# Performance work log

Measured on AMD Instinct MI355X. Metric: run time of the kernel, lower is better.

## Reference

```python
import jax, jax.numpy as jnp
import numpy as np


def _graph_conv_mean(x, src, dst, edge_weight, W_rel, W_root, b, num_nodes):
    # messages: gather source features, optionally scale by edge weight
    msg = x[src]  # [E, D]
    if edge_weight is not None:
        msg = msg * edge_weight[:, None]
    # mean aggregation over incoming edges per destination node
    summed = jax.ops.segment_sum(msg, dst, num_segments=num_nodes)  # [N, D]
    count = jax.ops.segment_sum(jnp.ones((src.shape[0],), x.dtype), dst, num_segments=num_nodes)
    mean = summed / jnp.maximum(count, 1.0)[:, None]
    # out = lin_rel(mean) + lin_root(x) + bias
    return mean @ W_rel + x @ W_root + b


def setup_inputs() -> dict:
    key = jax.random.key(0)
    ks = jax.random.split(key, 8)
    N, E, D, H, C = 100000, 1600000, 128, 32, 5
    x = jax.random.normal(ks[0], (N, D), dtype=jnp.float32)
    edge_index = jax.random.randint(ks[1], (2, E), 0, N, dtype=jnp.int64)
    edge_weight = jax.random.uniform(ks[2], (E,), dtype=jnp.float32)
    W_rel1 = jax.random.normal(ks[3], (D, H), dtype=jnp.float32) / np.sqrt(D)
    W_root1 = jax.random.normal(ks[4], (D, H), dtype=jnp.float32) / np.sqrt(D)
    b1 = jnp.zeros((H,), jnp.float32)
    W_rel2 = jax.random.normal(ks[5], (H, C), dtype=jnp.float32) / np.sqrt(H)
    W_root2 = jax.random.normal(ks[6], (H, C), dtype=jnp.float32) / np.sqrt(H)
    b2 = jnp.zeros((C,), jnp.float32)
    return {"x": x, "edge_index": edge_index, "edge_weight": edge_weight,
            "W_rel1": W_rel1, "W_root1": W_root1, "b1": b1,
            "W_rel2": W_rel2, "W_root2": W_root2, "b2": b2}


def reference(x, edge_index, edge_weight, W_rel1, W_root1, b1, W_rel2, W_root2, b2):
    N = x.shape[0]
    src, dst = edge_index[0], edge_index[1]
    # conv1 with edge_weight
    h = _graph_conv_mean(x, src, dst, edge_weight, W_rel1, W_root1, b1, N)
    h = jax.nn.relu(h)
    # dropout is identity at inference (training=False)
    # conv2 without edge_weight
    out = _graph_conv_mean(h, src, dst, None, W_rel2, W_root2, b2, N)
    return jax.nn.log_softmax(out, axis=1)
```

## Files before the change

kernel.cpp:

```cpp
#include <hip/hip_runtime.h>
#include <math.h>

#define N_NODES 100000
#define E_EDGES 1600000
#define D_IN    128
#define H_MID   32
#define C_OUT   5

#define BSHIFT 9
#define BNODES 512
#define NBKT   196
#define BCAP   9200
#define SRC_BITS 17
#define SRC_MASK 0x1FFFF

#define KP 136

typedef __attribute__((ext_vector_type(8))) short bf16x8;
typedef __attribute__((ext_vector_type(4))) float f32x4;

__device__ inline unsigned f2bf(float f) {
    unsigned u = __float_as_uint(f);
    return (u + 0x7FFFu + ((u >> 16) & 1u)) >> 16;
}

__global__ void k_prep(const float* __restrict__ Wrel,
                       const float* __restrict__ Wroot,
                       int* __restrict__ bucket_cursor,
                       unsigned short* __restrict__ wt_g) {
    int tid = threadIdx.x;
    bucket_cursor[tid] = 0;
    for (int i = tid; i < 64 * 128; i += 256) {
        int n = i >> 7, k = i & 127;
        float v = (n < H_MID) ? Wrel[k * H_MID + n] : Wroot[k * H_MID + (n - H_MID)];
        wt_g[i] = (unsigned short)f2bf(v);
    }
}

__global__ __launch_bounds__(256) void k1_mfma(
    const float* __restrict__ x,
    const unsigned short* __restrict__ wt_g,
    const float* __restrict__ b1,
    unsigned short* __restrict__ xrelh,
    float* __restrict__ xroot) {
    __shared__ unsigned short xs[64 * KP];
    int tid = threadIdx.x;
    int nodeBase = blockIdx.x * 64;

    #pragma unroll
    for (int it = 0; it < 16; ++it) {
        int idx = it * 256 + tid;
        int row = idx >> 6, kp = idx & 63;
        int node = nodeBase + row;
        float2 v = make_float2(0.f, 0.f);
        if (node < N_NODES)
            v = *(const float2*)(x + (size_t)node * D_IN + kp * 2);
        unsigned pk = f2bf(v.x) | (f2bf(v.y) << 16);
        *(unsigned*)(xs + row * KP + kp * 2) = pk;
    }
    __syncthreads();

    int lane = tid & 63;
    int wv = tid >> 6;
    int m = lane & 15;
    int quad = lane >> 4;

    f32x4 acc[4];
    #pragma unroll
    for (int nt = 0; nt < 4; ++nt) acc[nt] = (f32x4){0.f, 0.f, 0.f, 0.f};

    #pragma unroll
    for (int kk = 0; kk < 4; ++kk) {
        int k0 = kk * 32 + quad * 8;
        bf16x8 a = *(const bf16x8*)(xs + (wv * 16 + m) * KP + k0);
        #pragma unroll
        for (int nt = 0; nt < 4; ++nt) {
            bf16x8 b = *(const bf16x8*)(wt_g + (nt * 16 + m) * 128 + k0);
            acc[nt] = __builtin_amdgcn_mfma_f32_16x16x32_bf16(a, b, acc[nt], 0, 0, 0);
        }
    }

    #pragma unroll
    for (int nt = 0; nt < 4; ++nt) {
        #pragma unroll
        for (int r = 0; r < 4; ++r) {
            int node = nodeBase + wv * 16 + quad * 4 + r;
            int colg = nt * 16 + m;
            if (node < N_NODES) {
                if (colg < H_MID) {
                    xrelh[(size_t)node * H_MID + colg] =
                        (unsigned short)f2bf(acc[nt][r]);
                } else {
                    int c = colg - H_MID;
                    xroot[(size_t)node * H_MID + c] = acc[nt][r] + b1[c];
                }
            }
        }
    }
}

__global__ __launch_bounds__(1024) void k_binA(
    const int* __restrict__ src,
    const int* __restrict__ dst,
    const float* __restrict__ ew,
    int* __restrict__ bucket_cursor,
    int2* __restrict__ staged) {
    __shared__ int cnt[NBKT];
    __shared__ int lstart[NBKT];
    __shared__ int gbase[NBKT];
    __shared__ int scanbuf[256];
    __shared__ int2 ebuf[2048];
    __shared__ short bbuf[2048];
    int tid = threadIdx.x;
    int eBase = blockIdx.x * 2048;

    if (tid < NBKT) cnt[tid] = 0;
    __syncthreads();

    int b[2], rank[2], packed[2], wbits[2];
    bool valid[2];
    #pragma unroll
    for (int u = 0; u < 2; ++u) {
        int e = eBase + u * 1024 + tid;
        valid[u] = (e < E_EDGES);
        b[u] = 0; rank[u] = 0; packed[u] = 0; wbits[u] = 0;
        if (valid[u]) {
            int d = dst[e];
            int s = src[e];
            wbits[u] = __float_as_int(ew[e]);
            b[u] = d >> BSHIFT;
            packed[u] = ((d & (BNODES - 1)) << SRC_BITS) | s;
            rank[u] = atomicAdd(&cnt[b[u]], 1);
        }
    }
    __syncthreads();

    if (tid < 256) scanbuf[tid] = (tid < NBKT) ? cnt[tid] : 0;
    __syncthreads();
    for (int off = 1; off < 256; off <<= 1) {
        int t = 0;
        if (tid < 256 && tid >= off) t = scanbuf[tid - off];
        __syncthreads();
        if (tid < 256) scanbuf[tid] += t;
        __syncthreads();
    }
    if (tid < NBKT) {
        lstart[tid] = scanbuf[tid] - cnt[tid];
        gbase[tid]  = atomicAdd(&bucket_cursor[tid], cnt[tid]);
    }
    __syncthreads();
    int total = scanbuf[NBKT - 1];

    #pragma unroll
    for (int u = 0; u < 2; ++u) {
        if (valid[u]) {
            int slot = lstart[b[u]] + rank[u];
            ebuf[slot] = make_int2(packed[u], wbits[u]);
            bbuf[slot] = (short)b[u];
        }
    }
    __syncthreads();

    for (int t = tid; t < total; t += 1024) {
        int2 ev = ebuf[t];
        int bb = bbuf[t];
        int gpos = gbase[bb] + (t - lstart[bb]);
        if (gpos < BCAP)
            staged[(size_t)bb * BCAP + gpos] = ev;
    }
}

__global__ __launch_bounds__(1024) void k_binB2(
    const int* __restrict__ bucket_cursor,
    const int2* __restrict__ staged,
    int* __restrict__ deg,
    int* __restrict__ offsets,
    int2* __restrict__ csr8) {
    __shared__ int hist[BNODES];
    __shared__ int scanb[BNODES];
    __shared__ int cur[BNODES];
    __shared__ int sbase[256];
    int tid = threadIdx.x;
    int b = blockIdx.x;

    if (tid < 256) {
        int c = (tid < NBKT) ? bucket_cursor[tid] : 0;
        sbase[tid] = (c > BCAP) ? BCAP : c;
    }
    if (tid < BNODES) hist[tid] = 0;
    __syncthreads();
    for (int off = 1; off < 256; off <<= 1) {
        int t = 0;
        if (tid < 256 && tid >= off) t = sbase[tid - off];
        __syncthreads();
        if (tid < 256) sbase[tid] += t;
        __syncthreads();
    }
    int count = bucket_cursor[b];
    if (count > BCAP) count = BCAP;
    int base = sbase[b] - count;
    int nodeBase = b << BSHIFT;
    const int2* sp = staged + (size_t)b * BCAP;

    for (int i = tid; i < count; i += 1024)
        atomicAdd(&hist[((unsigned)sp[i].x) >> SRC_BITS], 1);
    __syncthreads();

    int v = 0;
    if (tid < BNODES) {
        v = hist[tid];
        scanb[tid] = v;
    }
    __syncthreads();
    for (int off = 1; off < BNODES; off <<= 1) {
        int t = 0;
        if (tid < BNODES && tid >= off) t = scanb[tid - off];
        __syncthreads();
        if (tid < BNODES) scanb[tid] += t;
        __syncthreads();
    }
    if (tid < BNODES) {
        int excl = scanb[tid] - v;
        int node = nodeBase + tid;
        if (node < N_NODES) {
            deg[node]     = v;
            offsets[node] = base + excl;
        }
        cur[tid] = excl;
    }
    __syncthreads();

    for (int i = tid; i < count; i += 1024) {
        int2 ev = sp[i];
        int local = ((unsigned)ev.x) >> SRC_BITS;
        int pos = atomicAdd(&cur[local], 1);
        csr8[base + pos] = make_int2(ev.x & SRC_MASK, ev.y);
    }
}

__global__ __launch_bounds__(512) void k_layer1(
    const int* __restrict__ offsets,
    const int* __restrict__ deg,
    const int2* __restrict__ csr8,
    const unsigned short* __restrict__ xrelh,
    const float* __restrict__ xroot,
    const float* __restrict__ Wrel2,
    const float* __restrict__ Wroot2,
    const float* __restrict__ b2,
    float* __restrict__ h2rel,
    float* __restrict__ h2root) {
    int node = blockIdx.x * 32 + (threadIdx.x >> 4);
    int lane = threadIdx.x & 15;
    int beg = offsets[node];
    int dg  = deg[node];
    int end = beg + dg;

    float acc0 = 0.f, acc1 = 0.f;
    int i = beg;
    for (; i + 8 <= end; i += 8) {
        int2 e[8];
        unsigned v[8];
        #pragma unroll
        for (int u = 0; u < 8; ++u) e[u] = csr8[i + u];
        #pragma unroll
        for (int u = 0; u < 8; ++u)
            v[u] = *(const unsigned*)(xrelh + (size_t)e[u].x * H_MID + lane * 2);
        #pragma unroll
        for (int u = 0; u < 8; ++u) {
            float w = __int_as_float(e[u].y);
            acc0 += __uint_as_float((v[u] & 0xFFFFu) << 16) * w;
            acc1 += __uint_as_float(v[u] & 0xFFFF0000u) * w;
        }
    }
    for (; i < end; ++i) {
        int2 e0 = csr8[i];
        unsigned v0 = *(const unsigned*)(xrelh + (size_t)e0.x * H_MID + lane * 2);
        float w0 = __int_as_float(e0.y);
        acc0 += __uint_as_float((v0 & 0xFFFFu) << 16) * w0;
        acc1 += __uint_as_float(v0 & 0xFFFF0000u) * w0;
    }

    float inv = 1.0f / fmaxf((float)dg, 1.0f);
    float2 rt = *(const float2*)(xroot + (size_t)node * H_MID + lane * 2);
    float h0 = fmaxf(acc0 * inv + rt.x, 0.f);
    float h1 = fmaxf(acc1 * inv + rt.y, 0.f);

    float p[2 * C_OUT];
    #pragma unroll
    for (int j = 0; j < C_OUT; ++j) {
        p[j]         = h0 * Wrel2[(2 * lane) * C_OUT + j]
                     + h1 * Wrel2[(2 * lane + 1) * C_OUT + j];
        p[C_OUT + j] = h0 * Wroot2[(2 * lane) * C_OUT + j]
                     + h1 * Wroot2[(2 * lane + 1) * C_OUT + j];
    }
    #pragma unroll
    for (int mm = 8; mm > 0; mm >>= 1) {
        #pragma unroll
        for (int j = 0; j < 2 * C_OUT; ++j)
            p[j] += __shfl_xor(p[j], mm, 16);
    }
    if (lane == 0) {
        #pragma unroll
        for (int j = 0; j < C_OUT; ++j) {
            h2rel[(size_t)node * C_OUT + j]  = p[j];
            h2root[(size_t)node * C_OUT + j] = p[C_OUT + j] + b2[j];
        }
    }
}

__global__ __launch_bounds__(256) void k_layer2(
    const int* __restrict__ offsets,
    const int* __restrict__ deg,
    const int2* __restrict__ csr8,
    const float* __restrict__ h2rel,
    const float* __restrict__ h2root,
    float* __restrict__ out) {
    int node = blockIdx.x * 32 + (threadIdx.x >> 3);
    int lane = threadIdx.x & 7;
    int beg = offsets[node];
    int dg  = deg[node];
    int end = beg + dg;

    float acc = 0.f;
    if (lane < C_OUT) {
        int i = beg;
        for (; i + 8 <= end; i += 8) {
            int s[8];
            float v[8];
            #pragma unroll
            for (int u = 0; u < 8; ++u) s[u] = csr8[i + u].x;
            #pragma unroll
            for (int u = 0; u < 8; ++u)
                v[u] = h2rel[(size_t)s[u] * C_OUT + lane];
            #pragma unroll
            for (int u = 0; u < 8; ++u) acc += v[u];
        }
        for (; i < end; ++i)
            acc += h2rel[(size_t)csr8[i].x * C_OUT + lane];
    }
    float inv = 1.0f / fmaxf((float)dg, 1.0f);
    float o = (lane < C_OUT)
                  ? acc * inv + h2root[(size_t)node * C_OUT + lane]
                  : -INFINITY;
    float m = o;
    #pragma unroll
    for (int dd = 4; dd > 0; dd >>= 1) m = fmaxf(m, __shfl_xor(m, dd, 8));
    float e = (lane < C_OUT) ? expf(o - m) : 0.f;
    float ssum = e;
    #pragma unroll
    for (int dd = 4; dd > 0; dd >>= 1) ssum += __shfl_xor(ssum, dd, 8);
    float lse = m + logf(ssum);
    if (lane < C_OUT)
        out[(size_t)node * C_OUT + lane] = o - lse;
}

extern "C" void kernel_launch(void* const* d_in, const int* in_sizes, int n_in,
                              void* d_out, int out_size, void* d_ws, size_t ws_size,
                              hipStream_t stream) {
    const float* x      = (const float*)d_in[0];
    const int*   ei     = (const int*)d_in[1];
    const float* ew     = (const float*)d_in[2];
    const float* Wrel1  = (const float*)d_in[3];
    const float* Wroot1 = (const float*)d_in[4];
    const float* b1     = (const float*)d_in[5];
    const float* Wrel2  = (const float*)d_in[6];
    const float* Wroot2 = (const float*)d_in[7];
    const float* b2     = (const float*)d_in[8];
    float* out = (float*)d_out;

    const int* src = ei;
    const int* dst = ei + E_EDGES;

    char* ws = (char*)d_ws;
    int*   deg           = (int*)ws;
    int*   bucket_cursor = deg + N_NODES;
    unsigned short* wt_g = (unsigned short*)(bucket_cursor + 256);
    int*   offsets       = (int*)(wt_g + 64 * 128);
    int2*  csr8          = (int2*)(offsets + N_NODES);
    unsigned short* xrelh = (unsigned short*)(csr8 + E_EDGES);
    float* xroot         = (float*)(xrelh + (size_t)N_NODES * H_MID);
    float* h2rel         = xroot + (size_t)N_NODES * H_MID;
    float* h2root        = h2rel + (size_t)N_NODES * C_OUT;
    int2*  staged        = (int2*)xrelh;

    k_prep<<<1, 256, 0, stream>>>(Wrel1, Wroot1, bucket_cursor, wt_g);

    k_binA<<<(E_EDGES + 2047) / 2048, 1024, 0, stream>>>(src, dst, ew,
                                                         bucket_cursor, staged);
    k_binB2<<<NBKT, 1024, 0, stream>>>(bucket_cursor, staged,
                                       deg, offsets, csr8);

    k1_mfma<<<(N_NODES + 63) / 64, 256, 0, stream>>>(x, wt_g, b1,
                                                     xrelh, xroot);

    k_layer1<<<N_NODES / 32, 512, 0, stream>>>(offsets, deg, csr8,
                                               xrelh, xroot, Wrel2, Wroot2, b2,
                                               h2rel, h2root);

    k_layer2<<<N_NODES / 32, 256, 0, stream>>>(offsets, deg, csr8,
                                               h2rel, h2root, out);
}
```

Before: 224.3 us.

## Fuse edge binning with node GEMM and aggregate per bucket from LDS CSR

Merges the edge-binning pass and the MFMA node-transform into one launch by splitting block ranges, and removes the global CSR build. Each layer kernel now re-sorts its bucket's staged edges into shared memory and aggregates directly from LDS, so the global csr/offset/deg arrays and one launch disappear. Bucket size halves to 256 nodes, giving 391 buckets and more blocks in the per-bucket kernels. The cost is that the per-bucket sort is done twice, once per layer, and the front kernel needs more shared memory per block with a wider scan.

```diff
diff --git a/kernel.cpp b/kernel.cpp
--- a/kernel.cpp
+++ b/kernel.cpp
@@ -7,12 +7,16 @@
 #define H_MID   32
 #define C_OUT   5
 
-#define BSHIFT 9
-#define BNODES 512
-#define NBKT   196
-#define BCAP   9200
+#define BSHIFT 8
+#define BNODES 256
+#define NBKT   391
+#define BCAP   4500
 #define SRC_BITS 17
 #define SRC_MASK 0x1FFFF
+
+#define EB     2048
+#define NBA    782
+#define NMF    782
 
 #define KP 136
 
@@ -23,6 +27,8 @@
     unsigned u = __float_as_uint(f);
     return (u + 0x7FFFu + ((u >> 16) & 1u)) >> 16;
 }
+__device__ inline float bflo(unsigned v) { return __uint_as_float((v & 0xFFFFu) << 16); }
+__device__ inline float bfhi(unsigned v) { return __uint_as_float(v & 0xFFFF0000u); }
 
 __global__ void k_prep(const float* __restrict__ Wrel,
                        const float* __restrict__ Wroot,
@@ -30,218 +36,152 @@
                        unsigned short* __restrict__ wt_g) {
     int tid = threadIdx.x;
     bucket_cursor[tid] = 0;
-    for (int i = tid; i < 64 * 128; i += 256) {
+    for (int i = tid; i < 64 * 128; i += 512) {
         int n = i >> 7, k = i & 127;
         float v = (n < H_MID) ? Wrel[k * H_MID + n] : Wroot[k * H_MID + (n - H_MID)];
         wt_g[i] = (unsigned short)f2bf(v);
     }
 }
 
-__global__ __launch_bounds__(256) void k1_mfma(
+__global__ __launch_bounds__(1024) void k_front(
+    const int* __restrict__ src,
+    const int* __restrict__ dst,
+    const float* __restrict__ ew,
+    int* __restrict__ bucket_cursor,
+    int2* __restrict__ staged,
     const float* __restrict__ x,
     const unsigned short* __restrict__ wt_g,
     const float* __restrict__ b1,
     unsigned short* __restrict__ xrelh,
     float* __restrict__ xroot) {
-    __shared__ unsigned short xs[64 * KP];
+    __shared__ __align__(16) char smem[128 * KP * 2];
     int tid = threadIdx.x;
-    int nodeBase = blockIdx.x * 64;
-
-    #pragma unroll
-    for (int it = 0; it < 16; ++it) {
-        int idx = it * 256 + tid;
-        int row = idx >> 6, kp = idx & 63;
-        int node = nodeBase + row;
-        float2 v = make_float2(0.f, 0.f);
-        if (node < N_NODES)
-            v = *(const float2*)(x + (size_t)node * D_IN + kp * 2);
-        unsigned pk = f2bf(v.x) | (f2bf(v.y) << 16);
-        *(unsigned*)(xs + row * KP + kp * 2) = pk;
-    }
-    __syncthreads();
-
-    int lane = tid & 63;
-    int wv = tid >> 6;
-    int m = lane & 15;
-    int quad = lane >> 4;
-
-    f32x4 acc[4];
-    #pragma unroll
-    for (int nt = 0; nt < 4; ++nt) acc[nt] = (f32x4){0.f, 0.f, 0.f, 0.f};
-
-    #pragma unroll
-    for (int kk = 0; kk < 4; ++kk) {
-        int k0 = kk * 32 + quad * 8;
-        bf16x8 a = *(const bf16x8*)(xs + (wv * 16 + m) * KP + k0);
-        #pragma unroll
-        for (int nt = 0; nt < 4; ++nt) {
-            bf16x8 b = *(const bf16x8*)(wt_g + (nt * 16 + m) * 128 + k0);
-            acc[nt] = __builtin_amdgcn_mfma_f32_16x16x32_bf16(a, b, acc[nt], 0, 0, 0);
-        }
-    }
-
-    #pragma unroll
-    for (int nt = 0; nt < 4; ++nt) {
-        #pragma unroll
-        for (int r = 0; r < 4; ++r) {
-            int node = nodeBase + wv * 16 + quad * 4 + r;
-            int colg = nt * 16 + m;
-            if (node < N_NODES) {
-                if (colg < H_MID) {
-                    xrelh[(size_t)node * H_MID + colg] =
-                        (unsigned short)f2bf(acc[nt][r]);
-                } else {
-                    int c = colg - H_MID;
-                    xroot[(size_t)node * H_MID + c] = acc[nt][r] + b1[c];
+
+    if (blockIdx.x < NBA) {
+        int2*  ebuf    = (int2*)smem;
+        short* bbuf    = (short*)(smem + 16384);
+        int*   cnt     = (int*)(smem + 20480);
+        int*   lstart  = (int*)(smem + 22080);
+        int*   gbase   = (int*)(smem + 23680);
+        int*   scanbuf = (int*)(smem + 25280);
+        int eBase = blockIdx.x * EB;
+
+        if (tid < NBKT) cnt[tid] = 0;
+        __syncthreads();
+
+        int b[2], rank[2], packed[2], wbits[2];
+        bool valid[2];
+        #pragma unroll
+        for (int u = 0; u < 2; ++u) {
+            int e = eBase + u * 1024 + tid;
+            valid[u] = (e < E_EDGES);
+            b[u] = 0; rank[u] = 0; packed[u] = 0; wbits[u] = 0;
+            if (valid[u]) {
+                int d = dst[e];
+                int s = src[e];
+                wbits[u] = __float_as_int(ew[e]);
+                b[u] = d >> BSHIFT;
+                packed[u] = ((d & (BNODES - 1)) << SRC_BITS) | s;
+                rank[u] = atomicAdd(&cnt[b[u]], 1);
+            }
+        }
+        __syncthreads();
+
+        if (tid < 512) scanbuf[tid] = (tid < NBKT) ? cnt[tid] : 0;
+        __syncthreads();
+        for (int off = 1; off < 512; off <<= 1) {
+            int t = 0;
+            if (tid < 512 && tid >= off) t = scanbuf[tid - off];
+            __syncthreads();
+            if (tid < 512) scanbuf[tid] += t;
+            __syncthreads();
+        }
+        if (tid < NBKT) {
+            lstart[tid] = scanbuf[tid] - cnt[tid];
+            gbase[tid]  = atomicAdd(&bucket_cursor[tid], cnt[tid]);
+        }
+        __syncthreads();
+        int total = scanbuf[NBKT - 1];
+
+        #pragma unroll
+        for (int u = 0; u < 2; ++u) {
+            if (valid[u]) {
+                int slot = lstart[b[u]] + rank[u];
+                ebuf[slot] = make_int2(packed[u], wbits[u]);
+                bbuf[slot] = (short)b[u];
+            }
+        }
+        __syncthreads();
+
+        for (int t = tid; t < total; t += 1024) {
+            int2 ev = ebuf[t];
+            int bb = bbuf[t];
+            int gpos = gbase[bb] + (t - lstart[bb]);
+            if (gpos < BCAP)
+                staged[(size_t)bb * BCAP + gpos] = ev;
+        }
+    } else {
+        unsigned short* xs = (unsigned short*)smem;
+        int nodeBase = (blockIdx.x - NBA) * 128;
+
+        #pragma unroll
+        for (int it = 0; it < 8; ++it) {
+            int idx = it * 1024 + tid;
+            int row = idx >> 6, kp = idx & 63;
+            int node = nodeBase + row;
+            float2 v = make_float2(0.f, 0.f);
+            if (node < N_NODES)
+                v = *(const float2*)(x + (size_t)node * D_IN + kp * 2);
+            unsigned pk = f2bf(v.x) | (f2bf(v.y) << 16);
+            *(unsigned*)(xs + row * KP + kp * 2) = pk;
+        }
+        __syncthreads();
+
+        int lane = tid & 63;
+        int wv = tid >> 6;
+        int m = lane & 15;
+        int quad = lane >> 4;
+        int rowBase = (wv & 7) * 16;
+        int ntBase = (wv >> 3) * 2;
+
+        f32x4 acc[2];
+        acc[0] = (f32x4){0.f, 0.f, 0.f, 0.f};
+        acc[1] = (f32x4){0.f, 0.f, 0.f, 0.f};
+
+        #pragma unroll
+        for (int kk = 0; kk < 4; ++kk) {
+            int k0 = kk * 32 + quad * 8;
+            bf16x8 a = *(const bf16x8*)(xs + (rowBase + m) * KP + k0);
+            #pragma unroll
+            for (int t = 0; t < 2; ++t) {
+                bf16x8 bb = *(const bf16x8*)(wt_g + ((ntBase + t) * 16 + m) * 128 + k0);
+                acc[t] = __builtin_amdgcn_mfma_f32_16x16x32_bf16(a, bb, acc[t], 0, 0, 0);
+            }
+        }
+
+        #pragma unroll
+        for (int t = 0; t < 2; ++t) {
+            #pragma unroll
+            for (int r = 0; r < 4; ++r) {
+                int node = nodeBase + rowBase + quad * 4 + r;
+                int colg = (ntBase + t) * 16 + m;
+                if (node < N_NODES) {
+                    if (colg < H_MID) {
+                        xrelh[(size_t)node * H_MID + colg] =
+                            (unsigned short)f2bf(acc[t][r]);
+                    } else {
+                        int c = colg - H_MID;
+                        xroot[(size_t)node * H_MID + c] = acc[t][r] + b1[c];
+                    }
                 }
             }
         }
     }
 }
 
-__global__ __launch_bounds__(1024) void k_binA(
-    const int* __restrict__ src,
-    const int* __restrict__ dst,
-    const float* __restrict__ ew,
-    int* __restrict__ bucket_cursor,
-    int2* __restrict__ staged) {
-    __shared__ int cnt[NBKT];
-    __shared__ int lstart[NBKT];
-    __shared__ int gbase[NBKT];
-    __shared__ int scanbuf[256];
-    __shared__ int2 ebuf[2048];
-    __shared__ short bbuf[2048];
-    int tid = threadIdx.x;
-    int eBase = blockIdx.x * 2048;
-
-    if (tid < NBKT) cnt[tid] = 0;
-    __syncthreads();
-
-    int b[2], rank[2], packed[2], wbits[2];
-    bool valid[2];
-    #pragma unroll
-    for (int u = 0; u < 2; ++u) {
-        int e = eBase + u * 1024 + tid;
-        valid[u] = (e < E_EDGES);
-        b[u] = 0; rank[u] = 0; packed[u] = 0; wbits[u] = 0;
-        if (valid[u]) {
-            int d = dst[e];
-            int s = src[e];
-            wbits[u] = __float_as_int(ew[e]);
-            b[u] = d >> BSHIFT;
-            packed[u] = ((d & (BNODES - 1)) << SRC_BITS) | s;
-            rank[u] = atomicAdd(&cnt[b[u]], 1);
-        }
-    }
-    __syncthreads();
-
-    if (tid < 256) scanbuf[tid] = (tid < NBKT) ? cnt[tid] : 0;
-    __syncthreads();
-    for (int off = 1; off < 256; off <<= 1) {
-        int t = 0;
-        if (tid < 256 && tid >= off) t = scanbuf[tid - off];
-        __syncthreads();
-        if (tid < 256) scanbuf[tid] += t;
-        __syncthreads();
-    }
-    if (tid < NBKT) {
-        lstart[tid] = scanbuf[tid] - cnt[tid];
-        gbase[tid]  = atomicAdd(&bucket_cursor[tid], cnt[tid]);
-    }
-    __syncthreads();
-    int total = scanbuf[NBKT - 1];
-
-    #pragma unroll
-    for (int u = 0; u < 2; ++u) {
-        if (valid[u]) {
-            int slot = lstart[b[u]] + rank[u];
-            ebuf[slot] = make_int2(packed[u], wbits[u]);
-            bbuf[slot] = (short)b[u];
-        }
-    }
-    __syncthreads();
-
-    for (int t = tid; t < total; t += 1024) {
-        int2 ev = ebuf[t];
-        int bb = bbuf[t];
-        int gpos = gbase[bb] + (t - lstart[bb]);
-        if (gpos < BCAP)
-            staged[(size_t)bb * BCAP + gpos] = ev;
-    }
-}
-
-__global__ __launch_bounds__(1024) void k_binB2(
+__global__ __launch_bounds__(1024) void k_bucket1(
     const int* __restrict__ bucket_cursor,
     const int2* __restrict__ staged,
-    int* __restrict__ deg,
-    int* __restrict__ offsets,
-    int2* __restrict__ csr8) {
-    __shared__ int hist[BNODES];
-    __shared__ int scanb[BNODES];
-    __shared__ int cur[BNODES];
-    __shared__ int sbase[256];
-    int tid = threadIdx.x;
-    int b = blockIdx.x;
-
-    if (tid < 256) {
-        int c = (tid < NBKT) ? bucket_cursor[tid] : 0;
-        sbase[tid] = (c > BCAP) ? BCAP : c;
-    }
-    if (tid < BNODES) hist[tid] = 0;
-    __syncthreads();
-    for (int off = 1; off < 256; off <<= 1) {
-        int t = 0;
-        if (tid < 256 && tid >= off) t = sbase[tid - off];
-        __syncthreads();
-        if (tid < 256) sbase[tid] += t;
-        __syncthreads();
-    }
-    int count = bucket_cursor[b];
-    if (count > BCAP) count = BCAP;
-    int base = sbase[b] - count;
-    int nodeBase = b << BSHIFT;
-    const int2* sp = staged + (size_t)b * BCAP;
-
-    for (int i = tid; i < count; i += 1024)
-        atomicAdd(&hist[((unsigned)sp[i].x) >> SRC_BITS], 1);
-    __syncthreads();
-
-    int v = 0;
-    if (tid < BNODES) {
-        v = hist[tid];
-        scanb[tid] = v;
-    }
-    __syncthreads();
-    for (int off = 1; off < BNODES; off <<= 1) {
-        int t = 0;
-        if (tid < BNODES && tid >= off) t = scanb[tid - off];
-        __syncthreads();
-        if (tid < BNODES) scanb[tid] += t;
-        __syncthreads();
-    }
-    if (tid < BNODES) {
-        int excl = scanb[tid] - v;
-        int node = nodeBase + tid;
-        if (node < N_NODES) {
-            deg[node]     = v;
-            offsets[node] = base + excl;
-        }
-        cur[tid] = excl;
-    }
-    __syncthreads();
-
-    for (int i = tid; i < count; i += 1024) {
-        int2 ev = sp[i];
-        int local = ((unsigned)ev.x) >> SRC_BITS;
-        int pos = atomicAdd(&cur[local], 1);
-        csr8[base + pos] = make_int2(ev.x & SRC_MASK, ev.y);
-    }
-}
-
-__global__ __launch_bounds__(512) void k_layer1(
-    const int* __restrict__ offsets,
-    const int* __restrict__ deg,
-    const int2* __restrict__ csr8,
     const unsigned short* __restrict__ xrelh,
     const float* __restrict__ xroot,
     const float* __restrict__ Wrel2,
@@ -249,109 +189,194 @@
     const float* __restrict__ b2,
     float* __restrict__ h2rel,
     float* __restrict__ h2root) {
-    int node = blockIdx.x * 32 + (threadIdx.x >> 4);
-    int lane = threadIdx.x & 15;
-    int beg = offsets[node];
-    int dg  = deg[node];
-    int end = beg + dg;
-
-    float acc0 = 0.f, acc1 = 0.f;
-    int i = beg;
-    for (; i + 8 <= end; i += 8) {
-        int2 e[8];
-        unsigned v[8];
-        #pragma unroll
-        for (int u = 0; u < 8; ++u) e[u] = csr8[i + u];
-        #pragma unroll
-        for (int u = 0; u < 8; ++u)
-            v[u] = *(const unsigned*)(xrelh + (size_t)e[u].x * H_MID + lane * 2);
-        #pragma unroll
-        for (int u = 0; u < 8; ++u) {
-            float w = __int_as_float(e[u].y);
-            acc0 += __uint_as_float((v[u] & 0xFFFFu) << 16) * w;
-            acc1 += __uint_as_float(v[u] & 0xFFFF0000u) * w;
-        }
-    }
-    for (; i < end; ++i) {
-        int2 e0 = csr8[i];
-        unsigned v0 = *(const unsigned*)(xrelh + (size_t)e0.x * H_MID + lane * 2);
-        float w0 = __int_as_float(e0.y);
-        acc0 += __uint_as_float((v0 & 0xFFFFu) << 16) * w0;
-        acc1 += __uint_as_float(v0 & 0xFFFF0000u) * w0;
-    }
-
-    float inv = 1.0f / fmaxf((float)dg, 1.0f);
-    float2 rt = *(const float2*)(xroot + (size_t)node * H_MID + lane * 2);
-    float h0 = fmaxf(acc0 * inv + rt.x, 0.f);
-    float h1 = fmaxf(acc1 * inv + rt.y, 0.f);
-
-    float p[2 * C_OUT];
-    #pragma unroll
-    for (int j = 0; j < C_OUT; ++j) {
-        p[j]         = h0 * Wrel2[(2 * lane) * C_OUT + j]
-                     + h1 * Wrel2[(2 * lane + 1) * C_OUT + j];
-        p[C_OUT + j] = h0 * Wroot2[(2 * lane) * C_OUT + j]
-                     + h1 * Wroot2[(2 * lane + 1) * C_OUT + j];
-    }
-    #pragma unroll
-    for (int mm = 8; mm > 0; mm >>= 1) {
-        #pragma unroll
-        for (int j = 0; j < 2 * C_OUT; ++j)
-            p[j] += __shfl_xor(p[j], mm, 16);
-    }
-    if (lane == 0) {
+    __shared__ int2 ecsr[BCAP];
+    __shared__ int hist[BNODES];
+    __shared__ int scanb[BNODES];
+    __shared__ int nstart[BNODES];
+    __shared__ int cur[BNODES];
+    int tid = threadIdx.x;
+    int b = blockIdx.x;
+
+    int count = bucket_cursor[b];
+    if (count > BCAP) count = BCAP;
+    const int2* sp = staged + (size_t)b * BCAP;
+
+    if (tid < BNODES) hist[tid] = 0;
+    __syncthreads();
+    for (int i = tid; i < count; i += 1024)
+        atomicAdd(&hist[((unsigned)sp[i].x) >> SRC_BITS], 1);
+    __syncthreads();
+
+    int v = 0;
+    if (tid < BNODES) { v = hist[tid]; scanb[tid] = v; }
+    __syncthreads();
+    for (int off = 1; off < BNODES; off <<= 1) {
+        int t = 0;
+        if (tid < BNODES && tid >= off) t = scanb[tid - off];
+        __syncthreads();
+        if (tid < BNODES) scanb[tid] += t;
+        __syncthreads();
+    }
+    if (tid < BNODES) {
+        int e0 = scanb[tid] - v;
+        nstart[tid] = e0;
+        cur[tid] = e0;
+    }
+    __syncthreads();
+
+    for (int i = tid; i < count; i += 1024) {
+        int2 ev = sp[i];
+        int local = ((unsigned)ev.x) >> SRC_BITS;
+        int pos = atomicAdd(&cur[local], 1);
+        ecsr[pos] = make_int2(ev.x & SRC_MASK, ev.y);
+    }
+    __syncthreads();
+
+    int g = tid >> 4;
+    int lane = tid & 15;
+    for (int nl = g; nl < BNODES; nl += 64) {
+        int node = b * BNODES + nl;
+        if (node >= N_NODES) continue;
+        int dg = hist[nl];
+        int i = nstart[nl];
+        int end = i + dg;
+
+        float acc0 = 0.f, acc1 = 0.f;
+        for (; i + 4 <= end; i += 4) {
+            int2 e0 = ecsr[i], e1 = ecsr[i + 1], e2 = ecsr[i + 2], e3 = ecsr[i + 3];
+            unsigned v0 = *(const unsigned*)(xrelh + (size_t)e0.x * H_MID + lane * 2);
+            unsigned v1 = *(const unsigned*)(xrelh + (size_t)e1.x * H_MID + lane * 2);
+            unsigned v2 = *(const unsigned*)(xrelh + (size_t)e2.x * H_MID + lane * 2);
+            unsigned v3 = *(const unsigned*)(xrelh + (size_t)e3.x * H_MID + lane * 2);
+            float w0 = __int_as_float(e0.y), w1 = __int_as_float(e1.y);
+            float w2 = __int_as_float(e2.y), w3 = __int_as_float(e3.y);
+            acc0 += bflo(v0) * w0; acc1 += bfhi(v0) * w0;
+            acc0 += bflo(v1) * w1; acc1 += bfhi(v1) * w1;
+            acc0 += bflo(v2) * w2; acc1 += bfhi(v2) * w2;
+            acc0 += bflo(v3) * w3; acc1 += bfhi(v3) * w3;
+        }
+        for (; i < end; ++i) {
+            int2 e0 = ecsr[i];
+            unsigned v0 = *(const unsigned*)(xrelh + (size_t)e0.x * H_MID + lane * 2);
+            float w0 = __int_as_float(e0.y);
+            acc0 += bflo(v0) * w0; acc1 += bfhi(v0) * w0;
+        }
+
+        float inv = 1.0f / fmaxf((float)dg, 1.0f);
+        float2 rt = *(const float2*)(xroot + (size_t)node * H_MID + lane * 2);
+        float h0 = fmaxf(acc0 * inv + rt.x, 0.f);
+        float h1 = fmaxf(acc1 * inv + rt.y, 0.f);
+
+        float p[2 * C_OUT];
         #pragma unroll
         for (int j = 0; j < C_OUT; ++j) {
-            h2rel[(size_t)node * C_OUT + j]  = p[j];
-            h2root[(size_t)node * C_OUT + j] = p[C_OUT + j] + b2[j];
-        }
-    }
-}
-
-__global__ __launch_bounds__(256) void k_layer2(
-    const int* __restrict__ offsets,
-    const int* __restrict__ deg,
-    const int2* __restrict__ csr8,
+            p[j]         = h0 * Wrel2[(2 * lane) * C_OUT + j]
+                         + h1 * Wrel2[(2 * lane + 1) * C_OUT + j];
+            p[C_OUT + j] = h0 * Wroot2[(2 * lane) * C_OUT + j]
+                         + h1 * Wroot2[(2 * lane + 1) * C_OUT + j];
+        }
+        #pragma unroll
+        for (int mm = 8; mm > 0; mm >>= 1) {
+            #pragma unroll
+            for (int j = 0; j < 2 * C_OUT; ++j)
+                p[j] += __shfl_xor(p[j], mm, 16);
+        }
+        if (lane == 0) {
+            #pragma unroll
+            for (int j = 0; j < C_OUT; ++j) {
+                h2rel[(size_t)node * C_OUT + j]  = p[j];
+                h2root[(size_t)node * C_OUT + j] = p[C_OUT + j] + b2[j];
+            }
+        }
+    }
+}
+
+__global__ __launch_bounds__(1024) void k_bucket2(
+    const int* __restrict__ bucket_cursor,
+    const int2* __restrict__ staged,
     const float* __restrict__ h2rel,
     const float* __restrict__ h2root,
     float* __restrict__ out) {
-    int node = blockIdx.x * 32 + (threadIdx.x >> 3);
-    int lane = threadIdx.x & 7;
-    int beg = offsets[node];
-    int dg  = deg[node];
-    int end = beg + dg;
-
-    float acc = 0.f;
-    if (lane < C_OUT) {
-        int i = beg;
-        for (; i + 8 <= end; i += 8) {
-            int s[8];
-            float v[8];
-            #pragma unroll
-            for (int u = 0; u < 8; ++u) s[u] = csr8[i + u].x;
-            #pragma unroll
-            for (int u = 0; u < 8; ++u)
-                v[u] = h2rel[(size_t)s[u] * C_OUT + lane];
-            #pragma unroll
-            for (int u = 0; u < 8; ++u) acc += v[u];
-        }
-        for (; i < end; ++i)
-            acc += h2rel[(size_t)csr8[i].x * C_OUT + lane];
-    }
-    float inv = 1.0f / fmaxf((float)dg, 1.0f);
-    float o = (lane < C_OUT)
-                  ? acc * inv + h2root[(size_t)node * C_OUT + lane]
-                  : -INFINITY;
-    float m = o;
-    #pragma unroll
-    for (int dd = 4; dd > 0; dd >>= 1) m = fmaxf(m, __shfl_xor(m, dd, 8));
-    float e = (lane < C_OUT) ? expf(o - m) : 0.f;
-    float ssum = e;
-    #pragma unroll
-    for (int dd = 4; dd > 0; dd >>= 1) ssum += __shfl_xor(ssum, dd, 8);
-    float lse = m + logf(ssum);
-    if (lane < C_OUT)
-        out[(size_t)node * C_OUT + lane] = o - lse;
+    __shared__ int esrc[BCAP];
+    __shared__ int hist[BNODES];
+    __shared__ int scanb[BNODES];
+    __shared__ int nstart[BNODES];
+    __shared__ int cur[BNODES];
+    int tid = threadIdx.x;
+    int b = blockIdx.x;
+
+    int count = bucket_cursor[b];
+    if (count > BCAP) count = BCAP;
+    const int2* sp = staged + (size_t)b * BCAP;
+
+    if (tid < BNODES) hist[tid] = 0;
+    __syncthreads();
+    for (int i = tid; i < count; i += 1024)
+        atomicAdd(&hist[((unsigned)sp[i].x) >> SRC_BITS], 1);
+    __syncthreads();
+
+    int v = 0;
+    if (tid < BNODES) { v = hist[tid]; scanb[tid] = v; }
+    __syncthreads();
+    for (int off = 1; off < BNODES; off <<= 1) {
+        int t = 0;
+        if (tid < BNODES && tid >= off) t = scanb[tid - off];
+        __syncthreads();
+        if (tid < BNODES) scanb[tid] += t;
+        __syncthreads();
+    }
+    if (tid < BNODES) {
+        int e0 = scanb[tid] - v;
+        nstart[tid] = e0;
+        cur[tid] = e0;
+    }
+    __syncthreads();
+
+    for (int i = tid; i < count; i += 1024) {
+        int ex = sp[i].x;
+        int local = ((unsigned)ex) >> SRC_BITS;
+        int pos = atomicAdd(&cur[local], 1);
+        esrc[pos] = ex & SRC_MASK;
+    }
+    __syncthreads();
+
+    int g = tid >> 3;
+    int lane = tid & 7;
+    for (int nl = g; nl < BNODES; nl += 128) {
+        int node = b * BNODES + nl;
+        if (node >= N_NODES) continue;
+        int dg = hist[nl];
+        int beg = nstart[nl];
+
+        float acc = 0.f;
+        if (lane < C_OUT) {
+            int i = beg, end = beg + dg;
+            for (; i + 4 <= end; i += 4) {
+                int s0 = esrc[i], s1 = esrc[i + 1], s2 = esrc[i + 2], s3 = esrc[i + 3];
+                float v0 = h2rel[(size_t)s0 * C_OUT + lane];
+                float v1 = h2rel[(size_t)s1 * C_OUT + lane];
+                float v2 = h2rel[(size_t)s2 * C_OUT + lane];
+                float v3 = h2rel[(size_t)s3 * C_OUT + lane];
+                acc += v0 + v1 + v2 + v3;
+            }
+            for (; i < end; ++i)
+                acc += h2rel[(size_t)esrc[i] * C_OUT + lane];
+        }
+        float inv = 1.0f / fmaxf((float)dg, 1.0f);
+        float o = (lane < C_OUT)
+                      ? acc * inv + h2root[(size_t)node * C_OUT + lane]
+                      : -INFINITY;
+        float m = o;
+        #pragma unroll
+        for (int dd = 4; dd > 0; dd >>= 1) m = fmaxf(m, __shfl_xor(m, dd, 8));
+        float e = (lane < C_OUT) ? expf(o - m) : 0.f;
+        float ssum = e;
+        #pragma unroll
+        for (int dd = 4; dd > 0; dd >>= 1) ssum += __shfl_xor(ssum, dd, 8);
+        float lse = m + logf(ssum);
+        if (lane < C_OUT)
+            out[(size_t)node * C_OUT + lane] = o - lse;
+    }
 }
 
 extern "C" void kernel_launch(void* const* d_in, const int* in_sizes, int n_in,
@@ -372,31 +397,23 @@
     const int* dst = ei + E_EDGES;
 
     char* ws = (char*)d_ws;
-    int*   deg           = (int*)ws;
-    int*   bucket_cursor = deg + N_NODES;
-    unsigned short* wt_g = (unsigned short*)(bucket_cursor + 256);
-    int*   offsets       = (int*)(wt_g + 64 * 128);
-    int2*  csr8          = (int2*)(offsets + N_NODES);
-    unsigned short* xrelh = (unsigned short*)(csr8 + E_EDGES);
+    int*   bucket_cursor = (int*)ws;
+    unsigned short* wt_g = (unsigned short*)(bucket_cursor + 512);
+    int2*  staged        = (int2*)(wt_g + 64 * 128);
+    unsigned short* xrelh = (unsigned short*)(staged + (size_t)NBKT * BCAP);
     float* xroot         = (float*)(xrelh + (size_t)N_NODES * H_MID);
     float* h2rel         = xroot + (size_t)N_NODES * H_MID;
     float* h2root        = h2rel + (size_t)N_NODES * C_OUT;
-    int2*  staged        = (int2*)xrelh;
-
-    k_prep<<<1, 256, 0, stream>>>(Wrel1, Wroot1, bucket_cursor, wt_g);
-
-    k_binA<<<(E_EDGES + 2047) / 2048, 1024, 0, stream>>>(src, dst, ew,
-                                                         bucket_cursor, staged);
-    k_binB2<<<NBKT, 1024, 0, stream>>>(bucket_cursor, staged,
-                                       deg, offsets, csr8);
-
-    k1_mfma<<<(N_NODES + 63) / 64, 256, 0, stream>>>(x, wt_g, b1,
-                                                     xrelh, xroot);
-
-    k_layer1<<<N_NODES / 32, 512, 0, stream>>>(offsets, deg, csr8,
-                                               xrelh, xroot, Wrel2, Wroot2, b2,
-                                               h2rel, h2root);
-
-    k_layer2<<<N_NODES / 32, 256, 0, stream>>>(offsets, deg, csr8,
-                                               h2rel, h2root, out);
-}
+
+    k_prep<<<1, 512, 0, stream>>>(Wrel1, Wroot1, bucket_cursor, wt_g);
+
+    k_front<<<NBA + NMF, 1024, 0, stream>>>(src, dst, ew, bucket_cursor, staged,
+                                            x, wt_g, b1, xrelh, xroot);
+
+    k_bucket1<<<NBKT, 1024, 0, stream>>>(bucket_cursor, staged,
+                                         xrelh, xroot, Wrel2, Wroot2, b2,
+                                         h2rel, h2root);
+
+    k_bucket2<<<NBKT, 1024, 0, stream>>>(bucket_cursor, staged,
+                                         h2rel, h2root, out);
+}
```

After: 206.3 us. 8.0% less time.
